# Kernel tuning notes

Measured on AMD Instinct MI355X. Metric: run time of the kernel, lower is better.

Reference implementation:

```python
import jax, jax.numpy as jnp
import numpy as np

QMAX = 127.0

def quantize_rowwise(a):
    """bnb-style vector-wise (per-row) absmax int8 quantization.
    Returns (q, scale) with q in [-127, 127] and a ~= q * scale."""
    absmax = jnp.max(jnp.abs(a), axis=-1, keepdims=True)
    scale = jnp.maximum(absmax, 1e-8) / QMAX          # per-row scale
    q = jnp.clip(jnp.round(a / scale), -QMAX, QMAX)   # int8 values (kept float)
    return q, scale

def setup_inputs() -> dict:
    key = jax.random.key(0)
    k1, k2, k3 = jax.random.split(key, 3)
    tokens, d_in, d_out = 8192, 4096, 4096
    x = jax.random.normal(k1, (tokens, d_in), dtype=jnp.float32)
    W = jax.random.normal(k2, (d_out, d_in), dtype=jnp.float32) * 0.02
    bias = jax.random.normal(k3, (d_out,), dtype=jnp.float32) * 0.01
    return {"x": x, "W": W, "bias": bias}

def reference(x, W, bias):
    # Linear8bitLt(has_fp16_weights=False):
    #   weight stored as int8 CB with per-output-channel absmax scale SCB,
    #   input quantized per-row to int8, int8xint8 -> int32 GEMM,
    #   dequant: acc * (scale_x outer scale_w), then + bias.
    qw, sw = quantize_rowwise(W)        # [d_out, d_in], [d_out, 1]
    qx, sx = quantize_rowwise(x)        # [T, d_in],     [T, 1]
    acc = jnp.einsum('ti,oi->to', qx, qw)      # int32 accumulator (emulated in fp32)
    out = acc * (sx * sw.T) + bias[None, :]    # dequantize + bias
    return out
```

## Files before the change

### kernel.cpp

```cpp
#include <hip/hip_runtime.h>

typedef __attribute__((ext_vector_type(4))) int int4v;
typedef __attribute__((ext_vector_type(4))) float float4v;

#define QMAX 127.0f

__global__ __launch_bounds__(256) void quant_rows_fused(
    const float* __restrict__ x, const float* __restrict__ w,
    signed char* __restrict__ qxp, signed char* __restrict__ qwp,
    float* __restrict__ sxp, float* __restrict__ swp,
    int T, int K)
{
    const int blk = blockIdx.x;
    const float* a;
    signed char* q;
    float* scale;
    int row;
    if (blk < T) { a = x; q = qxp; scale = sxp; row = blk; }
    else         { a = w; q = qwp; scale = swp; row = blk - T; }

    const int t = threadIdx.x;
    const float4v* ap = (const float4v*)(a + (size_t)row * K);

    float4v v[4];
#pragma unroll
    for (int i = 0; i < 4; ++i) v[i] = ap[t + 256 * i];

    float m = 0.f;
#pragma unroll
    for (int i = 0; i < 4; ++i) {
        m = fmaxf(m, fabsf(v[i].x));
        m = fmaxf(m, fabsf(v[i].y));
        m = fmaxf(m, fabsf(v[i].z));
        m = fmaxf(m, fabsf(v[i].w));
    }
#pragma unroll
    for (int off = 32; off > 0; off >>= 1)
        m = fmaxf(m, __shfl_down(m, off, 64));
    __shared__ float wmax[4];
    if ((t & 63) == 0) wmax[t >> 6] = m;
    __syncthreads();
    const float am = fmaxf(fmaxf(wmax[0], wmax[1]), fmaxf(wmax[2], wmax[3]));
    const float s = fmaxf(am, 1e-8f) / QMAX;
    if (t == 0) scale[row] = s;

    const double inv = 1.0 / (double)s;

    int* qrow = (int*)(q + (size_t)row * K);
#pragma unroll
    for (int i = 0; i < 4; ++i) {
        float r0f = (float)((double)v[i].x * inv);
        float r1f = (float)((double)v[i].y * inv);
        float r2f = (float)((double)v[i].z * inv);
        float r3f = (float)((double)v[i].w * inv);
        int b0 = (int)fminf(fmaxf(rintf(r0f), -QMAX), QMAX);
        int b1 = (int)fminf(fmaxf(rintf(r1f), -QMAX), QMAX);
        int b2 = (int)fminf(fmaxf(rintf(r2f), -QMAX), QMAX);
        int b3 = (int)fminf(fmaxf(rintf(r3f), -QMAX), QMAX);
        qrow[t + 256 * i] =
            (b0 & 0xff) | ((b1 & 0xff) << 8) | ((b2 & 0xff) << 16) | ((b3 & 0xff) << 24);
    }
}

__global__ __launch_bounds__(256, 2) void gemm_i8_kernel(
    const signed char* __restrict__ qx,
    const signed char* __restrict__ qw,
    const float* __restrict__ sx,
    const float* __restrict__ sw,
    const float* __restrict__ bias,
    float* __restrict__ out,
    int M, int N, int K)
{
    __shared__ signed char smA[2][128 * 64];
    __shared__ signed char smB[2][256 * 64];

    const int t = threadIdx.x;
    const int lane = t & 63;
    const int wave = t >> 6;

    const int nx = gridDim.x;
    const int nwg = nx * gridDim.y;
    const int bid = blockIdx.y * nx + blockIdx.x;
    const int cpx = nwg >> 3;
    const int swz = (bid & 7) * cpx + (bid >> 3);
    const int bm = swz / nx;
    const int bn = swz % nx;

    const int wm = (wave >> 1) * 64;
    const int wn = (wave & 1) * 128;

    int4v acc[4][8];
#pragma unroll
    for (int i = 0; i < 4; ++i)
#pragma unroll
        for (int j = 0; j < 8; ++j)
            acc[i][j] = (int4v)0;

    const int r0 = t >> 2;
    const int c_src = ((t & 3) - ((t >> 3) & 3) + 4) & 3;
    const signed char* gA0 = qx + (size_t)(bm * 128 + r0) * K + c_src * 16;
    const signed char* gA1 = gA0 + (size_t)64 * K;
    const signed char* gB0 = qw + (size_t)(bn * 256 + r0) * K + c_src * 16;
    const signed char* gB1 = gB0 + (size_t)64 * K;
    const signed char* gB2 = gB1 + (size_t)64 * K;
    const signed char* gB3 = gB2 + (size_t)64 * K;

    signed char* const lA_0 = smA[0] + wave * 1024;
    signed char* const lA_1 = smA[1] + wave * 1024;
    signed char* const lB_0 = smB[0] + wave * 1024;
    signed char* const lB_1 = smB[1] + wave * 1024;

#define STAGE(b) do {                                                                  \
        __builtin_amdgcn_global_load_lds((const void*)gA0, (void*)(lA_##b),         16, 0, 0); \
        __builtin_amdgcn_global_load_lds((const void*)gA1, (void*)(lA_##b + 4096),  16, 0, 0); \
        __builtin_amdgcn_global_load_lds((const void*)gB0, (void*)(lB_##b),         16, 0, 0); \
        __builtin_amdgcn_global_load_lds((const void*)gB1, (void*)(lB_##b + 4096),  16, 0, 0); \
        __builtin_amdgcn_global_load_lds((const void*)gB2, (void*)(lB_##b + 8192),  16, 0, 0); \
        __builtin_amdgcn_global_load_lds((const void*)gB3, (void*)(lB_##b + 12288), 16, 0, 0); \
        gA0 += 64; gA1 += 64; gB0 += 64; gB1 += 64; gB2 += 64; gB3 += 64;              \
    } while (0)

    const int l16 = lane & 15;
    const int kq = lane >> 4;
    const int cr = (kq + ((l16 >> 1) & 3)) & 3;
    const int offA = (wm + l16) * 64 + cr * 16;
    const int offB = (wn + l16) * 64 + cr * 16;

#define COMPUTE(b) do {                                                     \
        int4v aF[4], bF[8];                                                 \
        _Pragma("unroll")                                                   \
        for (int mi = 0; mi < 4; ++mi)                                      \
            aF[mi] = *(const int4v*)(&smA[b][0] + offA + mi * 1024);        \
        _Pragma("unroll")                                                   \
        for (int ni = 0; ni < 8; ++ni)                                      \
            bF[ni] = *(const int4v*)(&smB[b][0] + offB + ni * 1024);        \
        _Pragma("unroll")                                                   \
        for (int mi = 0; mi < 4; ++mi)                                      \
            _Pragma("unroll")                                               \
            for (int ni = 0; ni < 8; ++ni)                                  \
                acc[mi][ni] = __builtin_amdgcn_mfma_i32_16x16x64_i8(        \
                    aF[mi], bF[ni], acc[mi][ni], 0, 0, 0);                  \
    } while (0)

#define FENCE() asm volatile("" ::: "memory")

    const int KITER = K >> 6;

    STAGE(0);
    for (int kk = 0; kk < KITER; kk += 2) {
        STAGE(1);
        asm volatile("s_waitcnt vmcnt(6)" ::: "memory");
        __builtin_amdgcn_s_barrier();
        FENCE();
        COMPUTE(0);
        FENCE();
        __builtin_amdgcn_s_barrier();
        FENCE();
        if (kk + 2 < KITER) {
            STAGE(0);
            asm volatile("s_waitcnt vmcnt(6)" ::: "memory");
        } else {
            asm volatile("s_waitcnt vmcnt(0)" ::: "memory");
        }
        __builtin_amdgcn_s_barrier();
        FENCE();
        COMPUTE(1);
        FENCE();
        __builtin_amdgcn_s_barrier();
        FENCE();
    }
#undef STAGE
#undef COMPUTE
#undef FENCE

    const int col0 = lane & 15;
    const int row0 = (lane >> 4) * 4;
#pragma unroll
    for (int mi = 0; mi < 4; ++mi) {
#pragma unroll
        for (int r = 0; r < 4; ++r) {
            const int gm = bm * 128 + wm + mi * 16 + row0 + r;
            const float sxr = sx[gm];
            float* orow = out + (size_t)gm * N + bn * 256 + wn;
#pragma unroll
            for (int ni = 0; ni < 8; ++ni) {
                const int gn_local = ni * 16 + col0;
                const int gn = bn * 256 + wn + gn_local;
                orow[gn_local] = (float)acc[mi][ni][r] * (sxr * sw[gn]) + bias[gn];
            }
        }
    }
    (void)M;
}

extern "C" void kernel_launch(void* const* d_in, const int* in_sizes, int n_in,
                              void* d_out, int out_size, void* d_ws, size_t ws_size,
                              hipStream_t stream) {
    const float* x    = (const float*)d_in[0];
    const float* W    = (const float*)d_in[1];
    const float* bias = (const float*)d_in[2];
    float* out = (float*)d_out;

    const int dout = in_sizes[2];
    const int din  = in_sizes[1] / dout;
    const int T    = in_sizes[0] / din;

    signed char* qx = (signed char*)d_ws;
    signed char* qw = qx + (size_t)T * din;
    float* sx = (float*)(qw + (size_t)dout * din);
    float* sw = sx + T;

    quant_rows_fused<<<T + dout, 256, 0, stream>>>(x, W, qx, qw, sx, sw, T, din);

    dim3 grid(dout / 256, T / 128);
    gemm_i8_kernel<<<grid, 256, 0, stream>>>(qx, qw, sx, sw, bias, out, T, dout, din);

    (void)n_in; (void)out_size; (void)ws_size;
}
```

Measured before the change: 403.3 us.

## Enlarge GEMM tile to 256x256 with 8 waves and 4-stage LDS pipeline

The int8 GEMM moves from a 128x256 tile with 4 waves to a 256x256 tile with 8 waves (512 threads), using a 4-buffer LDS ring of 128 KB. Staging of the next tiles is split into A and B halves interleaved with two half-tile MFMA phases, and MFMA issue priority is raised with s_setprio. The aim is to raise arithmetic intensity per byte loaded and to overlap global-to-LDS copies with compute. In exchange the K loop is hardcoded to 64 iterations (K=4096), and the larger LDS footprint and register use may limit occupancy.

```diff
diff --git a/kernel.cpp b/kernel.cpp
--- a/kernel.cpp
+++ b/kernel.cpp
@@ -62,7 +62,7 @@
     }
 }
 
-__global__ __launch_bounds__(256, 2) void gemm_i8_kernel(
+__global__ __launch_bounds__(512, 2) void gemm_i8_kernel(
     const signed char* __restrict__ qx,
     const signed char* __restrict__ qw,
     const float* __restrict__ sx,
@@ -71,8 +71,7 @@
     float* __restrict__ out,
     int M, int N, int K)
 {
-    __shared__ signed char smA[2][128 * 64];
-    __shared__ signed char smB[2][256 * 64];
+    __shared__ signed char sm[4 * 32768];
 
     const int t = threadIdx.x;
     const int lane = t & 63;
@@ -86,38 +85,36 @@
     const int bm = swz / nx;
     const int bn = swz % nx;
 
-    const int wm = (wave >> 1) * 64;
-    const int wn = (wave & 1) * 128;
-
-    int4v acc[4][8];
-#pragma unroll
-    for (int i = 0; i < 4; ++i)
-#pragma unroll
-        for (int j = 0; j < 8; ++j)
+    const int wm = (wave >> 2) * 128;
+    const int wn = (wave & 3) * 64;
+
+    int4v acc[8][4];
+#pragma unroll
+    for (int i = 0; i < 8; ++i)
+#pragma unroll
+        for (int j = 0; j < 4; ++j)
             acc[i][j] = (int4v)0;
 
     const int r0 = t >> 2;
     const int c_src = ((t & 3) - ((t >> 3) & 3) + 4) & 3;
-    const signed char* gA0 = qx + (size_t)(bm * 128 + r0) * K + c_src * 16;
-    const signed char* gA1 = gA0 + (size_t)64 * K;
+    const signed char* gA0 = qx + (size_t)(bm * 256 + r0) * K + c_src * 16;
+    const signed char* gA1 = gA0 + (size_t)128 * K;
     const signed char* gB0 = qw + (size_t)(bn * 256 + r0) * K + c_src * 16;
-    const signed char* gB1 = gB0 + (size_t)64 * K;
-    const signed char* gB2 = gB1 + (size_t)64 * K;
-    const signed char* gB3 = gB2 + (size_t)64 * K;
-
-    signed char* const lA_0 = smA[0] + wave * 1024;
-    signed char* const lA_1 = smA[1] + wave * 1024;
-    signed char* const lB_0 = smB[0] + wave * 1024;
-    signed char* const lB_1 = smB[1] + wave * 1024;
-
-#define STAGE(b) do {                                                                  \
-        __builtin_amdgcn_global_load_lds((const void*)gA0, (void*)(lA_##b),         16, 0, 0); \
-        __builtin_amdgcn_global_load_lds((const void*)gA1, (void*)(lA_##b + 4096),  16, 0, 0); \
-        __builtin_amdgcn_global_load_lds((const void*)gB0, (void*)(lB_##b),         16, 0, 0); \
-        __builtin_amdgcn_global_load_lds((const void*)gB1, (void*)(lB_##b + 4096),  16, 0, 0); \
-        __builtin_amdgcn_global_load_lds((const void*)gB2, (void*)(lB_##b + 8192),  16, 0, 0); \
-        __builtin_amdgcn_global_load_lds((const void*)gB3, (void*)(lB_##b + 12288), 16, 0, 0); \
-        gA0 += 64; gA1 += 64; gB0 += 64; gB1 += 64; gB2 += 64; gB3 += 64;              \
+    const signed char* gB1 = gB0 + (size_t)128 * K;
+
+#define STAGE_A(Sb) do {                                                                   \
+        __builtin_amdgcn_global_load_lds((const void*)gA0,                                 \
+            (void*)(sm + (Sb) * 32768 + wave * 1024), 16, 0, 0);                           \
+        __builtin_amdgcn_global_load_lds((const void*)gA1,                                 \
+            (void*)(sm + (Sb) * 32768 + 8192 + wave * 1024), 16, 0, 0);                    \
+        gA0 += 64; gA1 += 64;                                                              \
+    } while (0)
+#define STAGE_B(Sb) do {                                                                   \
+        __builtin_amdgcn_global_load_lds((const void*)gB0,                                 \
+            (void*)(sm + (Sb) * 32768 + 16384 + wave * 1024), 16, 0, 0);                   \
+        __builtin_amdgcn_global_load_lds((const void*)gB1,                                 \
+            (void*)(sm + (Sb) * 32768 + 16384 + 8192 + wave * 1024), 16, 0, 0);            \
+        gB0 += 64; gB1 += 64;                                                              \
     } while (0)
 
     const int l16 = lane & 15;
@@ -126,64 +123,101 @@
     const int offA = (wm + l16) * 64 + cr * 16;
     const int offB = (wn + l16) * 64 + cr * 16;
 
-#define COMPUTE(b) do {                                                     \
-        int4v aF[4], bF[8];                                                 \
-        _Pragma("unroll")                                                   \
-        for (int mi = 0; mi < 4; ++mi)                                      \
-            aF[mi] = *(const int4v*)(&smA[b][0] + offA + mi * 1024);        \
-        _Pragma("unroll")                                                   \
-        for (int ni = 0; ni < 8; ++ni)                                      \
-            bF[ni] = *(const int4v*)(&smB[b][0] + offB + ni * 1024);        \
-        _Pragma("unroll")                                                   \
-        for (int mi = 0; mi < 4; ++mi)                                      \
-            _Pragma("unroll")                                               \
-            for (int ni = 0; ni < 8; ++ni)                                  \
-                acc[mi][ni] = __builtin_amdgcn_mfma_i32_16x16x64_i8(        \
-                    aF[mi], bF[ni], acc[mi][ni], 0, 0, 0);                  \
+    int4v aF[4], bF[4];
+#define LOAD_A(Bb, mb) do {                                                                \
+        _Pragma("unroll")                                                                  \
+        for (int mi2 = 0; mi2 < 4; ++mi2)                                                  \
+            aF[mi2] = *(const int4v*)(sm + (Bb) * 32768 + offA + ((mb) + mi2) * 1024);     \
+    } while (0)
+#define LOAD_B(Bb) do {                                                                    \
+        _Pragma("unroll")                                                                  \
+        for (int ni2 = 0; ni2 < 4; ++ni2)                                                  \
+            bF[ni2] = *(const int4v*)(sm + (Bb) * 32768 + 16384 + offB + ni2 * 1024);      \
+    } while (0)
+#define MFMA16(mb) do {                                                                    \
+        _Pragma("unroll")                                                                  \
+        for (int mi2 = 0; mi2 < 4; ++mi2)                                                  \
+            _Pragma("unroll")                                                              \
+            for (int ni2 = 0; ni2 < 4; ++ni2)                                              \
+                acc[(mb) + mi2][ni2] = __builtin_amdgcn_mfma_i32_16x16x64_i8(              \
+                    aF[mi2], bF[ni2], acc[(mb) + mi2][ni2], 0, 0, 0);                      \
     } while (0)
 
 #define FENCE() asm volatile("" ::: "memory")
-
-    const int KITER = K >> 6;
-
-    STAGE(0);
-    for (int kk = 0; kk < KITER; kk += 2) {
-        STAGE(1);
-        asm volatile("s_waitcnt vmcnt(6)" ::: "memory");
-        __builtin_amdgcn_s_barrier();
-        FENCE();
-        COMPUTE(0);
-        FENCE();
-        __builtin_amdgcn_s_barrier();
-        FENCE();
-        if (kk + 2 < KITER) {
-            STAGE(0);
-            asm volatile("s_waitcnt vmcnt(6)" ::: "memory");
-        } else {
-            asm volatile("s_waitcnt vmcnt(0)" ::: "memory");
-        }
-        __builtin_amdgcn_s_barrier();
-        FENCE();
-        COMPUTE(1);
-        FENCE();
-        __builtin_amdgcn_s_barrier();
-        FENCE();
-    }
-#undef STAGE
-#undef COMPUTE
+#define WAIT_LGKM0() do { asm volatile("s_waitcnt lgkmcnt(0)" ::: "memory");               \
+                          __builtin_amdgcn_sched_barrier(0); } while (0)
+#define VM4() asm volatile("s_waitcnt vmcnt(4)" ::: "memory")
+#define VM0() asm volatile("s_waitcnt vmcnt(0)" ::: "memory")
+
+#define TILE(Bb, Sb, DOST, ENDW) do {                                                      \
+                                                           \
+        LOAD_A(Bb, 0); LOAD_B(Bb);                                                         \
+        if (DOST) { STAGE_A(Sb); }                                                         \
+        FENCE();                                                                           \
+        __builtin_amdgcn_s_barrier();                                                      \
+        FENCE();                                                                           \
+        WAIT_LGKM0();                                                                      \
+        __builtin_amdgcn_s_setprio(1);                                                     \
+        MFMA16(0);                                                                         \
+        __builtin_amdgcn_s_setprio(0);                                                     \
+        FENCE();                                                                           \
+        __builtin_amdgcn_s_barrier();                                                      \
+        FENCE();                                                                           \
+                                         \
+        LOAD_A(Bb, 4);                                                                     \
+        if (DOST) { STAGE_B(Sb); }                                                         \
+        FENCE();                                                                           \
+        __builtin_amdgcn_s_barrier();                                                      \
+        FENCE();                                                                           \
+        WAIT_LGKM0();                                                                      \
+        __builtin_amdgcn_s_setprio(1);                                                     \
+        MFMA16(4);                                                                         \
+        __builtin_amdgcn_s_setprio(0);                                                     \
+        FENCE();                                                                           \
+        ENDW;                                           \
+        __builtin_amdgcn_s_barrier();                    \
+        FENCE();                                                                           \
+    } while (0)
+
+    STAGE_A(0); STAGE_B(0);
+    STAGE_A(1); STAGE_B(1);
+    VM4();
+    __builtin_amdgcn_s_barrier();
+    FENCE();
+
+    for (int kk = 0; kk < 60; kk += 4) {
+        TILE(0, 2, true, VM4());
+        TILE(1, 3, true, VM4());
+        TILE(2, 0, true, VM4());
+        TILE(3, 1, true, VM4());
+    }
+    TILE(0, 2, true, VM4());
+    TILE(1, 3, true, VM4());
+    TILE(2, 0, false, VM0());
+    TILE(3, 1, false, );
+
+#undef TILE
+#undef STAGE_A
+#undef STAGE_B
+#undef LOAD_A
+#undef LOAD_B
+#undef MFMA16
+#undef WAIT_LGKM0
+#undef VM4
+#undef VM0
 #undef FENCE
 
     const int col0 = lane & 15;
     const int row0 = (lane >> 4) * 4;
 #pragma unroll
-    for (int mi = 0; mi < 4; ++mi) {
+    for (int mi = 0; mi < 8; ++mi) {
 #pragma unroll
         for (int r = 0; r < 4; ++r) {
-            const int gm = bm * 128 + wm + mi * 16 + row0 + r;
+            const int gm = bm * 256 + wm + mi * 16 + row0 + r;
             const float sxr = sx[gm];
             float* orow = out + (size_t)gm * N + bn * 256 + wn;
 #pragma unroll
-            for (int ni = 0; ni < 8; ++ni) {
+            for (int ni = 0; ni < 4; ++ni) {
                 const int gn_local = ni * 16 + col0;
                 const int gn = bn * 256 + wn + gn_local;
                 orow[gn_local] = (float)acc[mi][ni][r] * (sxr * sw[gn]) + bias[gn];
@@ -212,8 +246,8 @@
 
     quant_rows_fused<<<T + dout, 256, 0, stream>>>(x, W, qx, qw, sx, sw, T, din);
 
-    dim3 grid(dout / 256, T / 128);
-    gemm_i8_kernel<<<grid, 256, 0, stream>>>(qx, qw, sx, sw, bias, out, T, dout, din);
+    dim3 grid(dout / 256, T / 256);
+    gemm_i8_kernel<<<grid, 512, 0, stream>>>(qx, qw, sx, sw, bias, out, T, dout, din);
 
     (void)n_in; (void)out_size; (void)ws_size;
 }
```

After: 388.7 us. -3.6%, faster.
